# Performance work log

Hardware: AMD Instinct MI355X
Metric: run time of the kernel (lower is better)

The kernel has to match this reference:

```python
import jax, jax.numpy as jnp
import numpy as np

N_DIM = 1024
HEAD_NUM = 16
HEAD_DIM = N_DIM // HEAD_NUM


def setup_inputs() -> dict:
    key = jax.random.key(0)
    ks = jax.random.split(key, 6)
    s = 1.0 / np.sqrt(N_DIM)
    return {
        "x": jax.random.normal(ks[0], (2, 2048, N_DIM), dtype=jnp.float32),
        "wq": jax.random.uniform(ks[1], (N_DIM, N_DIM), jnp.float32, -s, s),
        "wk": jax.random.uniform(ks[2], (N_DIM, N_DIM), jnp.float32, -s, s),
        "wv": jax.random.uniform(ks[3], (N_DIM, N_DIM), jnp.float32, -s, s),
        "wo": jax.random.uniform(ks[4], (N_DIM, N_DIM), jnp.float32, -s, s),
        "bo": jax.random.uniform(ks[5], (N_DIM,), jnp.float32, -s, s),
    }


def reference(x, wq, wk, wv, wo, bo):
    B, S, D = x.shape
    # torch Linear: y = x @ W.T
    def proj(w):
        return (x @ w.T).reshape(B, S, HEAD_NUM, HEAD_DIM).transpose(0, 2, 1, 3)  # [B,H,S,Dh]
    q, k, v = proj(wq), proj(wk), proj(wv)
    scale = 1.0 / np.sqrt(HEAD_DIM).astype(np.float32)
    scores = jnp.einsum("bhqd,bhkd->bhqk", q, k) * scale  # [B,H,S,S]
    attn = jax.nn.softmax(scores, axis=-1)
    y = jnp.einsum("bhqk,bhkd->bhqd", attn, v)  # [B,H,S,Dh]
    y = y.transpose(0, 2, 1, 3).reshape(B, S, D)
    return y @ wo.T + bo
```

## Files before the change

### kernel.cpp

```cpp
#include <hip/hip_runtime.h>
#include <math.h>

#define B_DIM 2
#define S_DIM 2048
#define D_DIM 1024
#define H_NUM 16
#define DH    64
#define M_DIM (B_DIM * S_DIM)

typedef __attribute__((ext_vector_type(8))) short short8;
typedef __attribute__((ext_vector_type(4))) short short4v;
typedef __attribute__((ext_vector_type(4))) float float4v;
typedef __attribute__((ext_vector_type(4))) unsigned short ushort4v;
typedef unsigned short ushort;

static __device__ __forceinline__ ushort f2bf(float f) {
    unsigned u = __float_as_uint(f);
    u += 0x7fffu + ((u >> 16) & 1u);
    return (ushort)(u >> 16);
}

static __device__ __forceinline__ float fexp2(float x) {
#if __has_builtin(__builtin_amdgcn_exp2f)
    return __builtin_amdgcn_exp2f(x);
#else
    return exp2f(x);
#endif
}

static __device__ __forceinline__ unsigned cvtpk_bf16(float lo, float hi) {
    unsigned r;
    asm("v_cvt_pk_bf16_f32 %0, %1, %2" : "=v"(r) : "v"(lo), "v"(hi));
    return r;
}

static __device__ __forceinline__ void gload_lds16(const void* g, void* l) {
    __builtin_amdgcn_global_load_lds(
        (const __attribute__((address_space(1))) void*)g,
        (__attribute__((address_space(3))) void*)l, 16, 0, 0);
}

__global__ __launch_bounds__(256)
void cast_all(const float* __restrict__ x,  const float* __restrict__ wq,
              const float* __restrict__ wk, const float* __restrict__ wv,
              const float* __restrict__ wo, ushort* __restrict__ dst)
{
    const int i = blockIdx.x * 256 + threadIdx.x;
    const float4* s;
    int off;
    if      (i < 1048576) { s = (const float4*)x;  off = 0;       }
    else if (i < 1310720) { s = (const float4*)wq; off = 1048576; }
    else if (i < 1572864) { s = (const float4*)wk; off = 1310720; }
    else if (i < 1835008) { s = (const float4*)wv; off = 1572864; }
    else                  { s = (const float4*)wo; off = 1835008; }
    const float4 v = s[i - off];
    ushort4v o;
    o[0] = f2bf(v.x); o[1] = f2bf(v.y); o[2] = f2bf(v.z); o[3] = f2bf(v.w);
    ((ushort4v*)dst)[i] = o;
}

__global__ __launch_bounds__(256)
void gemm_bf16(const ushort* __restrict__ A, const ushort* __restrict__ B,
               ushort* __restrict__ Qh, ushort* __restrict__ Kh,
               ushort* __restrict__ Vt, float* __restrict__ Of,
               const float* __restrict__ bias, int mode)
{
    __shared__ ushort Asm[128 * 32];
    __shared__ ushort Bsm[128 * 32];

    const int K  = 1024;
    const int n0 = blockIdx.x * 128;
    const int m0 = blockIdx.y * 128;
    const int t    = threadIdx.x;
    const int w    = t >> 6;
    const int lane = t & 63;
    const int n    = lane & 15;
    const int quad = lane >> 4;
    const int wm = w >> 1, wn = w & 1;

    const int srow = w * 32 + (lane >> 2);
    const int skel = (lane & 3) * 8;

    float4v acc[4][4];
#pragma unroll
    for (int mt = 0; mt < 4; ++mt)
#pragma unroll
        for (int nt = 0; nt < 4; ++nt) acc[mt][nt] = (float4v){0.f, 0.f, 0.f, 0.f};

    for (int kt = 0; kt < K; kt += 32) {
#pragma unroll
        for (int i = 0; i < 2; ++i) {
            gload_lds16(&A[(size_t)(m0 + srow + i * 16) * K + kt + skel],
                        &Asm[(w * 2 + i) * 512]);
            gload_lds16(&B[(size_t)(n0 + srow + i * 16) * K + kt + skel],
                        &Bsm[(w * 2 + i) * 512]);
        }
        __syncthreads();

        short8 af[4], bfr[4];
#pragma unroll
        for (int mt = 0; mt < 4; ++mt)
            af[mt] = *(const short8*)&Asm[(wm * 64 + mt * 16 + n) * 32 + quad * 8];
#pragma unroll
        for (int nt = 0; nt < 4; ++nt)
            bfr[nt] = *(const short8*)&Bsm[(wn * 64 + nt * 16 + n) * 32 + quad * 8];

#pragma unroll
        for (int mt = 0; mt < 4; ++mt)
#pragma unroll
            for (int nt = 0; nt < 4; ++nt)
                acc[mt][nt] = __builtin_amdgcn_mfma_f32_16x16x32_bf16(
                    af[mt], bfr[nt], acc[mt][nt], 0, 0, 0);
        __syncthreads();
    }

    if (mode == 0) {
        const int wid = n0 >> 10;
        ushort* dstQK = (wid == 0) ? Qh : Kh;
        const float qs = (wid == 0) ? 0.1803368801f : 1.0f;
#pragma unroll
        for (int mt = 0; mt < 4; ++mt) {
            const int m = m0 + wm * 64 + mt * 16 + quad * 4;
            const int b = m >> 11, s = m & (S_DIM - 1);
#pragma unroll
            for (int nt = 0; nt < 4; ++nt) {
                const int ng = (n0 & 1023) + wn * 64 + nt * 16 + n;
                const int h = ng >> 6, d = ng & 63;
                const int bh = b * H_NUM + h;
                if (wid < 2) {
#pragma unroll
                    for (int r = 0; r < 4; ++r)
                        dstQK[(((size_t)bh * S_DIM + s + r) << 6) + d] =
                            f2bf(acc[mt][nt][r] * qs);
                } else {
                    ushort4v p;
#pragma unroll
                    for (int r = 0; r < 4; ++r) p[r] = f2bf(acc[mt][nt][r]);
                    *(ushort4v*)&Vt[(((size_t)bh * DH + d) << 11) + s] = p;
                }
            }
        }
    } else {
#pragma unroll
        for (int mt = 0; mt < 4; ++mt) {
            const int m = m0 + wm * 64 + mt * 16 + quad * 4;
#pragma unroll
            for (int nt = 0; nt < 4; ++nt) {
                const int ng = n0 + wn * 64 + nt * 16 + n;
                const float bv = bias[ng];
#pragma unroll
                for (int r = 0; r < 4; ++r)
                    Of[(size_t)(m + r) * D_DIM + ng] = acc[mt][nt][r] + bv;
            }
        }
    }
}

__global__ __launch_bounds__(256)
void attn_mfma(const ushort* __restrict__ Qh, const ushort* __restrict__ Kh,
               const ushort* __restrict__ Vt, ushort* __restrict__ Yh)
{
    __shared__ ushort Ksm[2][64 * 64];
    __shared__ ushort Vsm[2][64 * 64];

    const int w    = threadIdx.x >> 6;
    const int lane = threadIdx.x & 63;
    const int n    = lane & 15;
    const int quad = lane >> 4;

    const int wave_id = blockIdx.x * 4 + w;
    const int bh    = wave_id >> 6;
    const int qbase = (wave_id & 63) * 32;
    const int b     = bh >> 4;
    const int h     = bh & (H_NUM - 1);

    const ushort* Qb = Qh + (((size_t)bh * S_DIM) << 6);
    const ushort* Kb = Kh + (((size_t)bh * S_DIM) << 6);
    const ushort* Vb = Vt + (((size_t)bh * DH) << 11);

    const int l8 = lane >> 3;
    const int sg = (lane & 7) ^ l8;

    short8 qa[2][2];
#pragma unroll
    for (int mt = 0; mt < 2; ++mt)
#pragma unroll
        for (int kc = 0; kc < 2; ++kc)
            qa[mt][kc] = *(const short8*)&Qb[((size_t)(qbase + mt * 16 + n) << 6) + kc * 32 + quad * 8];

    float4v O[2][4];
    float   mrow[2], lrow[2];
#pragma unroll
    for (int mt = 0; mt < 2; ++mt) {
#pragma unroll
        for (int nt = 0; nt < 4; ++nt) O[mt][nt] = (float4v){0.f, 0.f, 0.f, 0.f};
        mrow[mt] = -1e30f; lrow[mt] = 0.f;
    }

    const int fswz[2] = { ((0 * 4 + quad) ^ (n & 7)) * 8,
                          ((1 * 4 + quad) ^ (n & 7)) * 8 };
    const int h4 = (quad & 1) * 4;
    const int q2 = quad >> 1;
    int vswz[2][2];
#pragma unroll
    for (int kc = 0; kc < 2; ++kc)
#pragma unroll
        for (int cc = 0; cc < 2; ++cc)
            vswz[kc][cc] = (((4 * kc + 2 * cc + q2) ^ (n & 7)) << 3) + h4;

#pragma unroll
    for (int i = 0; i < 2; ++i) {
        gload_lds16(&Kb[(size_t)(w * 16 + i * 8 + l8) * 64 + sg * 8],
                    &Ksm[0][(w * 16 + i * 8) * 64]);
        gload_lds16(&Vb[(size_t)(w * 16 + i * 8 + l8) * 2048 + sg * 8],
                    &Vsm[0][(w * 16 + i * 8) * 64]);
    }

    for (int kb = 0; kb < S_DIM / 64; ++kb) {
        __syncthreads();
        const int cur = kb & 1;
        if (kb + 1 < S_DIM / 64) {
            const int key1 = (kb + 1) * 64;
            const int nxt  = cur ^ 1;
#pragma unroll
            for (int i = 0; i < 2; ++i) {
                gload_lds16(&Kb[(size_t)(key1 + w * 16 + i * 8 + l8) * 64 + sg * 8],
                            &Ksm[nxt][(w * 16 + i * 8) * 64]);
                gload_lds16(&Vb[(size_t)(w * 16 + i * 8 + l8) * 2048 + key1 + sg * 8],
                            &Vsm[nxt][(w * 16 + i * 8) * 64]);
            }
        }

        short8 kf[4][2];
#pragma unroll
        for (int ct = 0; ct < 4; ++ct)
#pragma unroll
            for (int kc = 0; kc < 2; ++kc)
                kf[ct][kc] = *(const short8*)&Ksm[cur][(ct * 16 + n) * 64 + fswz[kc]];

        float4v s[2][4];
        __builtin_amdgcn_s_setprio(1);
#pragma unroll
        for (int mt = 0; mt < 2; ++mt)
#pragma unroll
            for (int ct = 0; ct < 4; ++ct) {
                float4v a = (float4v){0.f, 0.f, 0.f, 0.f};
                a = __builtin_amdgcn_mfma_f32_16x16x32_bf16(kf[ct][0], qa[mt][0], a, 0, 0, 0);
                a = __builtin_amdgcn_mfma_f32_16x16x32_bf16(kf[ct][1], qa[mt][1], a, 0, 0, 0);
                s[mt][ct] = a;
            }
        __builtin_amdgcn_s_setprio(0);

        short8 vf[4][2];
#pragma unroll
        for (int nt = 0; nt < 4; ++nt) {
            const int rb = (nt * 16 + n) * 64;
#pragma unroll
            for (int kc = 0; kc < 2; ++kc) {
                const short4v g0 = *(const short4v*)&Vsm[cur][rb + vswz[kc][0]];
                const short4v g1 = *(const short4v*)&Vsm[cur][rb + vswz[kc][1]];
                vf[nt][kc] = __builtin_shufflevector(g0, g1, 0, 1, 2, 3, 4, 5, 6, 7);
            }
        }

#pragma unroll
        for (int mt = 0; mt < 2; ++mt) {
            float lm = s[mt][0][0];
#pragma unroll
            for (int ct = 0; ct < 4; ++ct)
#pragma unroll
                for (int r = 0; r < 4; ++r)
                    lm = fmaxf(lm, s[mt][ct][r]);
            lm = fmaxf(lm, __shfl_xor(lm, 16, 64));
            lm = fmaxf(lm, __shfl_xor(lm, 32, 64));

            const bool ev = lm > mrow[mt] + 8.0f;
            if (__any(ev)) {
                const float mnew  = ev ? lm : mrow[mt];
                const float alpha = fexp2(mrow[mt] - mnew);
                mrow[mt] = mnew;
                lrow[mt] *= alpha;
                const int ai = __float_as_int(alpha);
                float av[4];
#pragma unroll
                for (int r = 0; r < 4; ++r)
                    av[r] = __int_as_float(
                        __builtin_amdgcn_ds_bpermute(4 * (quad * 4 + r), ai));
#pragma unroll
                for (int nt = 0; nt < 4; ++nt)
#pragma unroll
                    for (int r = 0; r < 4; ++r) O[mt][nt][r] *= av[r];
            }

            float pv[4][4];
            float lsum = 0.f;
#pragma unroll
            for (int ct = 0; ct < 4; ++ct)
#pragma unroll
                for (int r = 0; r < 4; ++r) {
                    const float p = fexp2(s[mt][ct][r] - mrow[mt]);
                    pv[ct][r] = p;
                    lsum += p;
                }
            lrow[mt] += lsum;

            union { unsigned u[4]; short8 s8; } pk[2];
#pragma unroll
            for (int kc = 0; kc < 2; ++kc) {
                pk[kc].u[0] = cvtpk_bf16(pv[2 * kc][0],     pv[2 * kc][1]);
                pk[kc].u[1] = cvtpk_bf16(pv[2 * kc][2],     pv[2 * kc][3]);
                pk[kc].u[2] = cvtpk_bf16(pv[2 * kc + 1][0], pv[2 * kc + 1][1]);
                pk[kc].u[3] = cvtpk_bf16(pv[2 * kc + 1][2], pv[2 * kc + 1][3]);
            }

            __builtin_amdgcn_s_setprio(1);
#pragma unroll
            for (int nt = 0; nt < 4; ++nt) {
                O[mt][nt] = __builtin_amdgcn_mfma_f32_16x16x32_bf16(pk[0].s8, vf[nt][0], O[mt][nt], 0, 0, 0);
                O[mt][nt] = __builtin_amdgcn_mfma_f32_16x16x32_bf16(pk[1].s8, vf[nt][1], O[mt][nt], 0, 0, 0);
            }
            __builtin_amdgcn_s_setprio(0);
        }
    }

#pragma unroll
    for (int mt = 0; mt < 2; ++mt) {
        float ls = lrow[mt];
        ls += __shfl_xor(ls, 16, 64);
        ls += __shfl_xor(ls, 32, 64);
        const float linv = 1.f / ls;
        const int  li = __float_as_int(linv);
        float lv[4];
#pragma unroll
        for (int r = 0; r < 4; ++r)
            lv[r] = __int_as_float(
                __builtin_amdgcn_ds_bpermute(4 * (quad * 4 + r), li));
#pragma unroll
        for (int nt = 0; nt < 4; ++nt)
#pragma unroll
            for (int r = 0; r < 4; ++r) {
                const int q = qbase + mt * 16 + quad * 4 + r;
                Yh[((size_t)(b * S_DIM + q) << 10) + h * DH + nt * 16 + n] =
                    f2bf(O[mt][nt][r] * lv[r]);
            }
    }
}

extern "C" void kernel_launch(void* const* d_in, const int* in_sizes, int n_in,
                              void* d_out, int out_size, void* d_ws, size_t ws_size,
                              hipStream_t stream)
{
    const float* x  = (const float*)d_in[0];
    const float* wq = (const float*)d_in[1];
    const float* wk = (const float*)d_in[2];
    const float* wv = (const float*)d_in[3];
    const float* wo = (const float*)d_in[4];
    const float* bo = (const float*)d_in[5];
    float* out = (float*)d_out;

    const size_t MD = (size_t)M_DIM * D_DIM;
    const size_t WD = (size_t)D_DIM * D_DIM;
    ushort* xh  = (ushort*)d_ws;
    ushort* Wh  = xh + MD;
    ushort* Woh = Wh + 3 * WD;
    ushort* Qh  = Woh + WD;
    ushort* Kh  = Qh + MD;
    ushort* Vt  = Kh + MD;
    ushort* Yh  = Vt + MD;
    if (ws_size < 48u * 1024u * 1024u) return;

    dim3 blk(256);
    cast_all<<<dim3(8192), blk, 0, stream>>>(x, wq, wk, wv, wo, xh);

    gemm_bf16<<<dim3(24, 32), blk, 0, stream>>>(xh, Wh, Qh, Kh, Vt, nullptr, nullptr, 0);
    attn_mfma<<<dim3(512), blk, 0, stream>>>(Qh, Kh, Vt, Yh);
    gemm_bf16<<<dim3(8, 32), blk, 0, stream>>>(Yh, Woh, nullptr, nullptr, nullptr, out, bo, 1);
}
```

Measured before the change: 217.7 us.

## Compute softmax row sums via MFMA with ones and split output GEMM tiles

The attention kernel now accumulates the softmax denominator with an extra MFMA against a vector of bf16 ones, replacing the scalar per-lane sums, the final cross-lane shuffles and the bpermute broadcast. The row sum therefore lands in the same accumulator layout as O. The output projection moves to a dedicated kernel with 128x64 tiles, which doubles the block count from 256 to 512 for better CU occupancy. The max reduction is also restructured into a tree. Costs: two extra MFMAs per tile, and the row sums now come from bf16-rounded probabilities.

```diff
diff --git a/kernel.cpp b/kernel.cpp
--- a/kernel.cpp
+++ b/kernel.cpp
@@ -62,8 +62,7 @@
 __global__ __launch_bounds__(256)
 void gemm_bf16(const ushort* __restrict__ A, const ushort* __restrict__ B,
                ushort* __restrict__ Qh, ushort* __restrict__ Kh,
-               ushort* __restrict__ Vt, float* __restrict__ Of,
-               const float* __restrict__ bias, int mode)
+               ushort* __restrict__ Vt)
 {
     __shared__ ushort Asm[128 * 32];
     __shared__ ushort Bsm[128 * 32];
@@ -114,44 +113,95 @@
         __syncthreads();
     }
 
-    if (mode == 0) {
-        const int wid = n0 >> 10;
-        ushort* dstQK = (wid == 0) ? Qh : Kh;
-        const float qs = (wid == 0) ? 0.1803368801f : 1.0f;
-#pragma unroll
-        for (int mt = 0; mt < 4; ++mt) {
-            const int m = m0 + wm * 64 + mt * 16 + quad * 4;
-            const int b = m >> 11, s = m & (S_DIM - 1);
-#pragma unroll
-            for (int nt = 0; nt < 4; ++nt) {
-                const int ng = (n0 & 1023) + wn * 64 + nt * 16 + n;
-                const int h = ng >> 6, d = ng & 63;
-                const int bh = b * H_NUM + h;
-                if (wid < 2) {
-#pragma unroll
-                    for (int r = 0; r < 4; ++r)
-                        dstQK[(((size_t)bh * S_DIM + s + r) << 6) + d] =
-                            f2bf(acc[mt][nt][r] * qs);
-                } else {
-                    ushort4v p;
-#pragma unroll
-                    for (int r = 0; r < 4; ++r) p[r] = f2bf(acc[mt][nt][r]);
-                    *(ushort4v*)&Vt[(((size_t)bh * DH + d) << 11) + s] = p;
-                }
-            }
-        }
-    } else {
-#pragma unroll
-        for (int mt = 0; mt < 4; ++mt) {
-            const int m = m0 + wm * 64 + mt * 16 + quad * 4;
-#pragma unroll
-            for (int nt = 0; nt < 4; ++nt) {
-                const int ng = n0 + wn * 64 + nt * 16 + n;
-                const float bv = bias[ng];
+    const int wid = n0 >> 10;
+    ushort* dstQK = (wid == 0) ? Qh : Kh;
+    const float qs = (wid == 0) ? 0.1803368801f : 1.0f;
+#pragma unroll
+    for (int mt = 0; mt < 4; ++mt) {
+        const int m = m0 + wm * 64 + mt * 16 + quad * 4;
+        const int b = m >> 11, s = m & (S_DIM - 1);
+#pragma unroll
+        for (int nt = 0; nt < 4; ++nt) {
+            const int ng = (n0 & 1023) + wn * 64 + nt * 16 + n;
+            const int h = ng >> 6, d = ng & 63;
+            const int bh = b * H_NUM + h;
+            if (wid < 2) {
 #pragma unroll
                 for (int r = 0; r < 4; ++r)
-                    Of[(size_t)(m + r) * D_DIM + ng] = acc[mt][nt][r] + bv;
-            }
+                    dstQK[(((size_t)bh * S_DIM + s + r) << 6) + d] =
+                        f2bf(acc[mt][nt][r] * qs);
+            } else {
+                ushort4v p;
+#pragma unroll
+                for (int r = 0; r < 4; ++r) p[r] = f2bf(acc[mt][nt][r]);
+                *(ushort4v*)&Vt[(((size_t)bh * DH + d) << 11) + s] = p;
+            }
+        }
+    }
+}
+
+__global__ __launch_bounds__(256)
+void gemm_out(const ushort* __restrict__ A, const ushort* __restrict__ B,
+              float* __restrict__ Of, const float* __restrict__ bias)
+{
+    __shared__ ushort Asm[128 * 32];
+    __shared__ ushort Bsm[64 * 32];
+
+    const int K  = 1024;
+    const int n0 = blockIdx.x * 64;
+    const int m0 = blockIdx.y * 128;
+    const int t    = threadIdx.x;
+    const int w    = t >> 6;
+    const int lane = t & 63;
+    const int n    = lane & 15;
+    const int quad = lane >> 4;
+    const int wm = w >> 1, wn = w & 1;
+
+    const int srow  = w * 32 + (lane >> 2);
+    const int srowB = w * 16 + (lane >> 2);
+    const int skel  = (lane & 3) * 8;
+
+    float4v acc[4][2];
+#pragma unroll
+    for (int mt = 0; mt < 4; ++mt)
+#pragma unroll
+        for (int nt = 0; nt < 2; ++nt) acc[mt][nt] = (float4v){0.f, 0.f, 0.f, 0.f};
+
+    for (int kt = 0; kt < K; kt += 32) {
+#pragma unroll
+        for (int i = 0; i < 2; ++i)
+            gload_lds16(&A[(size_t)(m0 + srow + i * 16) * K + kt + skel],
+                        &Asm[(w * 2 + i) * 512]);
+        gload_lds16(&B[(size_t)(n0 + srowB) * K + kt + skel], &Bsm[w * 512]);
+        __syncthreads();
+
+        short8 af[4], bfr[2];
+#pragma unroll
+        for (int mt = 0; mt < 4; ++mt)
+            af[mt] = *(const short8*)&Asm[(wm * 64 + mt * 16 + n) * 32 + quad * 8];
+#pragma unroll
+        for (int nt = 0; nt < 2; ++nt)
+            bfr[nt] = *(const short8*)&Bsm[(wn * 32 + nt * 16 + n) * 32 + quad * 8];
+
+#pragma unroll
+        for (int mt = 0; mt < 4; ++mt)
+#pragma unroll
+            for (int nt = 0; nt < 2; ++nt)
+                acc[mt][nt] = __builtin_amdgcn_mfma_f32_16x16x32_bf16(
+                    af[mt], bfr[nt], acc[mt][nt], 0, 0, 0);
+        __syncthreads();
+    }
+
+#pragma unroll
+    for (int mt = 0; mt < 4; ++mt) {
+        const int m = m0 + wm * 64 + mt * 16 + quad * 4;
+#pragma unroll
+        for (int nt = 0; nt < 2; ++nt) {
+            const int ng = n0 + wn * 32 + nt * 16 + n;
+            const float bv = bias[ng];
+#pragma unroll
+            for (int r = 0; r < 4; ++r)
+                Of[(size_t)(m + r) * D_DIM + ng] = acc[mt][nt][r] + bv;
         }
     }
 }
@@ -188,13 +238,19 @@
         for (int kc = 0; kc < 2; ++kc)
             qa[mt][kc] = *(const short8*)&Qb[((size_t)(qbase + mt * 16 + n) << 6) + kc * 32 + quad * 8];
 
+    short8 ones;
+#pragma unroll
+    for (int e = 0; e < 8; ++e) ones[e] = (short)0x3F80;
+
     float4v O[2][4];
-    float   mrow[2], lrow[2];
+    float4v Ol[2];
+    float   mrow[2];
 #pragma unroll
     for (int mt = 0; mt < 2; ++mt) {
 #pragma unroll
         for (int nt = 0; nt < 4; ++nt) O[mt][nt] = (float4v){0.f, 0.f, 0.f, 0.f};
-        mrow[mt] = -1e30f; lrow[mt] = 0.f;
+        Ol[mt] = (float4v){0.f, 0.f, 0.f, 0.f};
+        mrow[mt] = -1e30f;
     }
 
     const int fswz[2] = { ((0 * 4 + quad) ^ (n & 7)) * 8,
@@ -265,12 +321,12 @@
 
 #pragma unroll
         for (int mt = 0; mt < 2; ++mt) {
-            float lm = s[mt][0][0];
+            float cmx[4];
 #pragma unroll
             for (int ct = 0; ct < 4; ++ct)
-#pragma unroll
-                for (int r = 0; r < 4; ++r)
-                    lm = fmaxf(lm, s[mt][ct][r]);
+                cmx[ct] = fmaxf(fmaxf(s[mt][ct][0], s[mt][ct][1]),
+                                fmaxf(s[mt][ct][2], s[mt][ct][3]));
+            float lm = fmaxf(fmaxf(cmx[0], cmx[1]), fmaxf(cmx[2], cmx[3]));
             lm = fmaxf(lm, __shfl_xor(lm, 16, 64));
             lm = fmaxf(lm, __shfl_xor(lm, 32, 64));
 
@@ -279,7 +335,6 @@
                 const float mnew  = ev ? lm : mrow[mt];
                 const float alpha = fexp2(mrow[mt] - mnew);
                 mrow[mt] = mnew;
-                lrow[mt] *= alpha;
                 const int ai = __float_as_int(alpha);
                 float av[4];
 #pragma unroll
@@ -290,19 +345,16 @@
                 for (int nt = 0; nt < 4; ++nt)
 #pragma unroll
                     for (int r = 0; r < 4; ++r) O[mt][nt][r] *= av[r];
+#pragma unroll
+                for (int r = 0; r < 4; ++r) Ol[mt][r] *= av[r];
             }
 
             float pv[4][4];
-            float lsum = 0.f;
 #pragma unroll
             for (int ct = 0; ct < 4; ++ct)
 #pragma unroll
-                for (int r = 0; r < 4; ++r) {
-                    const float p = fexp2(s[mt][ct][r] - mrow[mt]);
-                    pv[ct][r] = p;
-                    lsum += p;
-                }
-            lrow[mt] += lsum;
+                for (int r = 0; r < 4; ++r)
+                    pv[ct][r] = fexp2(s[mt][ct][r] - mrow[mt]);
 
             union { unsigned u[4]; short8 s8; } pk[2];
 #pragma unroll
@@ -319,30 +371,23 @@
                 O[mt][nt] = __builtin_amdgcn_mfma_f32_16x16x32_bf16(pk[0].s8, vf[nt][0], O[mt][nt], 0, 0, 0);
                 O[mt][nt] = __builtin_amdgcn_mfma_f32_16x16x32_bf16(pk[1].s8, vf[nt][1], O[mt][nt], 0, 0, 0);
             }
+            Ol[mt] = __builtin_amdgcn_mfma_f32_16x16x32_bf16(pk[0].s8, ones, Ol[mt], 0, 0, 0);
+            Ol[mt] = __builtin_amdgcn_mfma_f32_16x16x32_bf16(pk[1].s8, ones, Ol[mt], 0, 0, 0);
             __builtin_amdgcn_s_setprio(0);
         }
     }
 
 #pragma unroll
     for (int mt = 0; mt < 2; ++mt) {
-        float ls = lrow[mt];
-        ls += __shfl_xor(ls, 16, 64);
-        ls += __shfl_xor(ls, 32, 64);
-        const float linv = 1.f / ls;
-        const int  li = __float_as_int(linv);
-        float lv[4];
-#pragma unroll
-        for (int r = 0; r < 4; ++r)
-            lv[r] = __int_as_float(
-                __builtin_amdgcn_ds_bpermute(4 * (quad * 4 + r), li));
-#pragma unroll
-        for (int nt = 0; nt < 4; ++nt)
-#pragma unroll
-            for (int r = 0; r < 4; ++r) {
-                const int q = qbase + mt * 16 + quad * 4 + r;
+#pragma unroll
+        for (int r = 0; r < 4; ++r) {
+            const float linv = 1.f / Ol[mt][r];
+            const int q = qbase + mt * 16 + quad * 4 + r;
+#pragma unroll
+            for (int nt = 0; nt < 4; ++nt)
                 Yh[((size_t)(b * S_DIM + q) << 10) + h * DH + nt * 16 + n] =
-                    f2bf(O[mt][nt][r] * lv[r]);
-            }
+                    f2bf(O[mt][nt][r] * linv);
+        }
     }
 }
 
@@ -372,7 +417,7 @@
     dim3 blk(256);
     cast_all<<<dim3(8192), blk, 0, stream>>>(x, wq, wk, wv, wo, xh);
 
-    gemm_bf16<<<dim3(24, 32), blk, 0, stream>>>(xh, Wh, Qh, Kh, Vt, nullptr, nullptr, 0);
+    gemm_bf16<<<dim3(24, 32), blk, 0, stream>>>(xh, Wh, Qh, Kh, Vt);
     attn_mfma<<<dim3(512), blk, 0, stream>>>(Qh, Kh, Vt, Yh);
-    gemm_bf16<<<dim3(8, 32), blk, 0, stream>>>(Yh, Woh, nullptr, nullptr, nullptr, out, bo, 1);
-}
+    gemm_out<<<dim3(16, 32), blk, 0, stream>>>(Yh, Woh, out, bo);
+}
```

Result: no change. 217.2 us (-0.2%).

## Deepen GEMM K-tile to 64 with XOR-swizzled LDS and block swizzle

Applied to the files above, without the earlier changes.

Both GEMMs now load a 64-wide K slice per iteration, halving the number of barrier pairs. The LDS layout is XOR-swizzled on both the global-to-LDS writes and the fragment reads to avoid bank conflicts. Blocks are remapped with a grouped swizzle so neighbouring blocks share operand tiles in L2. The output projection gets a dedicated kernel with a 128x64 tile, giving 512 blocks instead of 256 to fill more CUs, at the cost of less reuse per block and double the LDS footprint.

```diff
diff --git a/kernel.cpp b/kernel.cpp
--- a/kernel.cpp
+++ b/kernel.cpp
@@ -62,15 +62,16 @@
 __global__ __launch_bounds__(256)
 void gemm_bf16(const ushort* __restrict__ A, const ushort* __restrict__ B,
                ushort* __restrict__ Qh, ushort* __restrict__ Kh,
-               ushort* __restrict__ Vt, float* __restrict__ Of,
-               const float* __restrict__ bias, int mode)
+               ushort* __restrict__ Vt)
 {
-    __shared__ ushort Asm[128 * 32];
-    __shared__ ushort Bsm[128 * 32];
-
-    const int K  = 1024;
-    const int n0 = blockIdx.x * 128;
-    const int m0 = blockIdx.y * 128;
+    __shared__ ushort Asm[128 * 64];
+    __shared__ ushort Bsm[128 * 64];
+
+    const int K = 1024;
+    const int lin = blockIdx.y * 24 + blockIdx.x;
+    const int swz = (lin & 7) * 96 + (lin >> 3);
+    const int n0 = (swz % 24) * 128;
+    const int m0 = (swz / 24) * 128;
     const int t    = threadIdx.x;
     const int w    = t >> 6;
     const int lane = t & 63;
@@ -78,8 +79,11 @@
     const int quad = lane >> 4;
     const int wm = w >> 1, wn = w & 1;
 
-    const int srow = w * 32 + (lane >> 2);
-    const int skel = (lane & 3) * 8;
+    const int l8 = lane >> 3;
+    const int sg = (lane & 7) ^ l8;
+
+    const int fswz[2] = { ((0 * 4 + quad) ^ (n & 7)) * 8,
+                          ((1 * 4 + quad) ^ (n & 7)) * 8 };
 
     float4v acc[4][4];
 #pragma unroll
@@ -87,71 +91,142 @@
 #pragma unroll
         for (int nt = 0; nt < 4; ++nt) acc[mt][nt] = (float4v){0.f, 0.f, 0.f, 0.f};
 
-    for (int kt = 0; kt < K; kt += 32) {
-#pragma unroll
-        for (int i = 0; i < 2; ++i) {
-            gload_lds16(&A[(size_t)(m0 + srow + i * 16) * K + kt + skel],
-                        &Asm[(w * 2 + i) * 512]);
-            gload_lds16(&B[(size_t)(n0 + srow + i * 16) * K + kt + skel],
-                        &Bsm[(w * 2 + i) * 512]);
+    for (int kt = 0; kt < K; kt += 64) {
+#pragma unroll
+        for (int i = 0; i < 4; ++i) {
+            gload_lds16(&A[(size_t)(m0 + w * 32 + i * 8 + l8) * K + kt + sg * 8],
+                        &Asm[(w * 32 + i * 8) * 64]);
+            gload_lds16(&B[(size_t)(n0 + w * 32 + i * 8 + l8) * K + kt + sg * 8],
+                        &Bsm[(w * 32 + i * 8) * 64]);
         }
         __syncthreads();
 
-        short8 af[4], bfr[4];
+        short8 af[4][2], bfr[4][2];
 #pragma unroll
         for (int mt = 0; mt < 4; ++mt)
-            af[mt] = *(const short8*)&Asm[(wm * 64 + mt * 16 + n) * 32 + quad * 8];
+#pragma unroll
+            for (int kk = 0; kk < 2; ++kk)
+                af[mt][kk] = *(const short8*)&Asm[(wm * 64 + mt * 16 + n) * 64 + fswz[kk]];
 #pragma unroll
         for (int nt = 0; nt < 4; ++nt)
-            bfr[nt] = *(const short8*)&Bsm[(wn * 64 + nt * 16 + n) * 32 + quad * 8];
+#pragma unroll
+            for (int kk = 0; kk < 2; ++kk)
+                bfr[nt][kk] = *(const short8*)&Bsm[(wn * 64 + nt * 16 + n) * 64 + fswz[kk]];
 
 #pragma unroll
         for (int mt = 0; mt < 4; ++mt)
 #pragma unroll
-            for (int nt = 0; nt < 4; ++nt)
+            for (int nt = 0; nt < 4; ++nt) {
                 acc[mt][nt] = __builtin_amdgcn_mfma_f32_16x16x32_bf16(
-                    af[mt], bfr[nt], acc[mt][nt], 0, 0, 0);
+                    af[mt][0], bfr[nt][0], acc[mt][nt], 0, 0, 0);
+                acc[mt][nt] = __builtin_amdgcn_mfma_f32_16x16x32_bf16(
+                    af[mt][1], bfr[nt][1], acc[mt][nt], 0, 0, 0);
+            }
         __syncthreads();
     }
 
-    if (mode == 0) {
-        const int wid = n0 >> 10;
-        ushort* dstQK = (wid == 0) ? Qh : Kh;
-        const float qs = (wid == 0) ? 0.1803368801f : 1.0f;
-#pragma unroll
-        for (int mt = 0; mt < 4; ++mt) {
-            const int m = m0 + wm * 64 + mt * 16 + quad * 4;
-            const int b = m >> 11, s = m & (S_DIM - 1);
-#pragma unroll
-            for (int nt = 0; nt < 4; ++nt) {
-                const int ng = (n0 & 1023) + wn * 64 + nt * 16 + n;
-                const int h = ng >> 6, d = ng & 63;
-                const int bh = b * H_NUM + h;
-                if (wid < 2) {
-#pragma unroll
-                    for (int r = 0; r < 4; ++r)
-                        dstQK[(((size_t)bh * S_DIM + s + r) << 6) + d] =
-                            f2bf(acc[mt][nt][r] * qs);
-                } else {
-                    ushort4v p;
-#pragma unroll
-                    for (int r = 0; r < 4; ++r) p[r] = f2bf(acc[mt][nt][r]);
-                    *(ushort4v*)&Vt[(((size_t)bh * DH + d) << 11) + s] = p;
-                }
-            }
-        }
-    } else {
-#pragma unroll
-        for (int mt = 0; mt < 4; ++mt) {
-            const int m = m0 + wm * 64 + mt * 16 + quad * 4;
-#pragma unroll
-            for (int nt = 0; nt < 4; ++nt) {
-                const int ng = n0 + wn * 64 + nt * 16 + n;
-                const float bv = bias[ng];
+    const int wid = n0 >> 10;
+    ushort* dstQK = (wid == 0) ? Qh : Kh;
+    const float qs = (wid == 0) ? 0.1803368801f : 1.0f;
+#pragma unroll
+    for (int mt = 0; mt < 4; ++mt) {
+        const int m = m0 + wm * 64 + mt * 16 + quad * 4;
+        const int b = m >> 11, s = m & (S_DIM - 1);
+#pragma unroll
+        for (int nt = 0; nt < 4; ++nt) {
+            const int ng = (n0 & 1023) + wn * 64 + nt * 16 + n;
+            const int h = ng >> 6, d = ng & 63;
+            const int bh = b * H_NUM + h;
+            if (wid < 2) {
 #pragma unroll
                 for (int r = 0; r < 4; ++r)
-                    Of[(size_t)(m + r) * D_DIM + ng] = acc[mt][nt][r] + bv;
-            }
+                    dstQK[(((size_t)bh * S_DIM + s + r) << 6) + d] =
+                        f2bf(acc[mt][nt][r] * qs);
+            } else {
+                ushort4v p;
+#pragma unroll
+                for (int r = 0; r < 4; ++r) p[r] = f2bf(acc[mt][nt][r]);
+                *(ushort4v*)&Vt[(((size_t)bh * DH + d) << 11) + s] = p;
+            }
+        }
+    }
+}
+
+__global__ __launch_bounds__(256)
+void gemm_out(const ushort* __restrict__ A, const ushort* __restrict__ B,
+              float* __restrict__ Of, const float* __restrict__ bias)
+{
+    __shared__ ushort Asm[128 * 64];
+    __shared__ ushort Bsm[64 * 64];
+
+    const int K = 1024;
+    const int lin = blockIdx.y * 16 + blockIdx.x;
+    const int swz = (lin & 7) * 64 + (lin >> 3);
+    const int n0 = (swz % 16) * 64;
+    const int m0 = (swz / 16) * 128;
+    const int t    = threadIdx.x;
+    const int w    = t >> 6;
+    const int lane = t & 63;
+    const int n    = lane & 15;
+    const int quad = lane >> 4;
+    const int wm = w >> 1, wn = w & 1;
+
+    const int l8 = lane >> 3;
+    const int sg = (lane & 7) ^ l8;
+    const int fswz[2] = { ((0 * 4 + quad) ^ (n & 7)) * 8,
+                          ((1 * 4 + quad) ^ (n & 7)) * 8 };
+
+    float4v acc[4][2];
+#pragma unroll
+    for (int mt = 0; mt < 4; ++mt)
+#pragma unroll
+        for (int nt = 0; nt < 2; ++nt) acc[mt][nt] = (float4v){0.f, 0.f, 0.f, 0.f};
+
+    for (int kt = 0; kt < K; kt += 64) {
+#pragma unroll
+        for (int i = 0; i < 4; ++i)
+            gload_lds16(&A[(size_t)(m0 + w * 32 + i * 8 + l8) * K + kt + sg * 8],
+                        &Asm[(w * 32 + i * 8) * 64]);
+#pragma unroll
+        for (int i = 0; i < 2; ++i)
+            gload_lds16(&B[(size_t)(n0 + w * 16 + i * 8 + l8) * K + kt + sg * 8],
+                        &Bsm[(w * 16 + i * 8) * 64]);
+        __syncthreads();
+
+        short8 af[4][2], bfr[2][2];
+#pragma unroll
+        for (int mt = 0; mt < 4; ++mt)
+#pragma unroll
+            for (int kk = 0; kk < 2; ++kk)
+                af[mt][kk] = *(const short8*)&Asm[(wm * 64 + mt * 16 + n) * 64 + fswz[kk]];
+#pragma unroll
+        for (int nt = 0; nt < 2; ++nt)
+#pragma unroll
+            for (int kk = 0; kk < 2; ++kk)
+                bfr[nt][kk] = *(const short8*)&Bsm[(wn * 32 + nt * 16 + n) * 64 + fswz[kk]];
+
+#pragma unroll
+        for (int mt = 0; mt < 4; ++mt)
+#pragma unroll
+            for (int nt = 0; nt < 2; ++nt) {
+                acc[mt][nt] = __builtin_amdgcn_mfma_f32_16x16x32_bf16(
+                    af[mt][0], bfr[nt][0], acc[mt][nt], 0, 0, 0);
+                acc[mt][nt] = __builtin_amdgcn_mfma_f32_16x16x32_bf16(
+                    af[mt][1], bfr[nt][1], acc[mt][nt], 0, 0, 0);
+            }
+        __syncthreads();
+    }
+
+#pragma unroll
+    for (int mt = 0; mt < 4; ++mt) {
+        const int m = m0 + wm * 64 + mt * 16 + quad * 4;
+#pragma unroll
+        for (int nt = 0; nt < 2; ++nt) {
+            const int ng = n0 + wn * 32 + nt * 16 + n;
+            const float bv = bias[ng];
+#pragma unroll
+            for (int r = 0; r < 4; ++r)
+                Of[(size_t)(m + r) * D_DIM + ng] = acc[mt][nt][r] + bv;
         }
     }
 }
@@ -372,7 +447,7 @@
     dim3 blk(256);
     cast_all<<<dim3(8192), blk, 0, stream>>>(x, wq, wk, wv, wo, xh);
 
-    gemm_bf16<<<dim3(24, 32), blk, 0, stream>>>(xh, Wh, Qh, Kh, Vt, nullptr, nullptr, 0);
+    gemm_bf16<<<dim3(24, 32), blk, 0, stream>>>(xh, Wh, Qh, Kh, Vt);
     attn_mfma<<<dim3(512), blk, 0, stream>>>(Qh, Kh, Vt, Yh);
-    gemm_bf16<<<dim3(8, 32), blk, 0, stream>>>(Yh, Woh, nullptr, nullptr, nullptr, out, bo, 1);
-}
+    gemm_out<<<dim3(16, 32), blk, 0, stream>>>(Yh, Woh, out, bo);
+}
```

Measured after the change: 207.8 us. -4.5%, faster.
